# Optimization experiments

Measured on AMD Instinct MI355X. Metric: run time of the kernel, lower is better.

## Reference

```python
import jax, jax.numpy as jnp
import numpy as np

N_NODES = 50000
FEAT = 128
FP_LEN = 2048
RADIUS = 4
N_EDGES = 600000
BN_EPS = 1e-5


def setup_inputs() -> dict:
    key = jax.random.key(0)
    ks = jax.random.split(key, 8)
    s_h = 1.0 / np.sqrt(FEAT)  # torch Linear default init scale
    return {
        "atoms_features": jax.random.normal(ks[0], (N_NODES, FEAT), jnp.float32),
        "edge_index": jax.random.randint(ks[1], (2, N_EDGES), 0, N_NODES, dtype=jnp.int64),
        "init_w": jax.random.normal(ks[2], (FEAT, FP_LEN), jnp.float32) * s_h,
        "init_b": jnp.zeros((FP_LEN,), jnp.float32),
        "hash_w": jax.random.normal(ks[3], (RADIUS, FEAT, FEAT), jnp.float32) * s_h,
        "hash_b": jnp.zeros((RADIUS, FEAT), jnp.float32),
        "soft_w": jax.random.normal(ks[4], (RADIUS, FEAT, FP_LEN), jnp.float32) * s_h,
        "soft_b": jnp.zeros((RADIUS, FP_LEN), jnp.float32),
        "bn_gamma": jnp.ones((FEAT,), jnp.float32),
        "bn_beta": jnp.zeros((FEAT,), jnp.float32),
    }


def reference(atoms_features, edge_index, init_w, init_b, hash_w, hash_b,
              soft_w, soft_b, bn_gamma, bn_beta):
    n = atoms_features.shape[0]
    src, dst = edge_index[0], edge_index[1]

    # initial soft assignment: fingerprint += sum_atoms softmax(W x + b)
    fp = jnp.sum(jax.nn.softmax(atoms_features @ init_w + init_b, axis=1), axis=0)

    feats = atoms_features
    for l in range(RADIUS):
        # neighbor-sum aggregation: self + sum of neighbor features (scatter-add over edges)
        agg = feats + jax.ops.segment_sum(feats[src], dst, num_segments=n)
        # hash: Linear -> ReLU -> BatchNorm (training-mode batch stats, biased var)
        h = jax.nn.relu(agg @ hash_w[l] + hash_b[l])
        mu = jnp.mean(h, axis=0)
        var = jnp.mean(jnp.square(h - mu), axis=0)
        h = (h - mu) * jax.lax.rsqrt(var + BN_EPS) * bn_gamma + bn_beta
        # soft assignment contribution
        fp = fp + jnp.sum(jax.nn.softmax(h @ soft_w[l] + soft_b[l], axis=1), axis=0)
        # original round-trips through numpy between layers -> detach
        feats = jax.lax.stop_gradient(h)

    return fp[None, :]  # [1, FP_LEN]
```

## Files before the change

kernel.cpp:

```cpp
#include <hip/hip_runtime.h>
#include <hip/hip_bf16.h>

#define N_NODES 50000
#define FEAT    128
#define FP_LEN  2048
#define RADIUS  4
#define N_EDGES 600000
#define BN_EPS  1e-5f
#define SM_ROWS 16

__global__ __launch_bounds__(256) void k_zero(float* fp, float* stats,
                                              int* counts, int* cursor) {
    int i = blockIdx.x * blockDim.x + threadIdx.x;
    int n = gridDim.x * blockDim.x;
    for (int j = i; j < FP_LEN; j += n) fp[j] = 0.f;
    for (int j = i; j < RADIUS * 2 * FEAT; j += n) stats[j] = 0.f;
    for (int j = i; j < N_NODES; j += n) { counts[j] = 0; cursor[j] = 0; }
}

__global__ __launch_bounds__(256) void k_count(const int* __restrict__ dst,
                                               int* __restrict__ counts) {
    int e = blockIdx.x * 256 + threadIdx.x;
    if (e < N_EDGES) {
        unsigned d = (unsigned)dst[e];
        if (d < N_NODES) atomicAdd(&counts[d], 1);
    }
}

__global__ __launch_bounds__(1024) void k_scan(const int* __restrict__ counts,
                                               int* __restrict__ offs) {
    __shared__ int part[1024];
    int tid = threadIdx.x;
    const int chunk = (N_NODES + 1023) / 1024;
    int lo = tid * chunk;
    int hi = min(lo + chunk, N_NODES);
    int s = 0;
    for (int i = lo; i < hi; i++) s += counts[i];
    part[tid] = s;
    __syncthreads();
    for (int off = 1; off < 1024; off <<= 1) {
        int v = (tid >= off) ? part[tid - off] : 0;
        __syncthreads();
        part[tid] += v;
        __syncthreads();
    }
    int run = part[tid] - s;
    for (int i = lo; i < hi; i++) { offs[i] = run; run += counts[i]; }
    if (lo < N_NODES && hi == N_NODES) offs[N_NODES] = run;
}

__global__ __launch_bounds__(256) void k_fill(const int* __restrict__ src,
                                              const int* __restrict__ dst,
                                              const int* __restrict__ offs,
                                              int* __restrict__ cursor,
                                              int* __restrict__ csr) {
    int e = blockIdx.x * 256 + threadIdx.x;
    if (e < N_EDGES) {
        unsigned d = (unsigned)dst[e];
        unsigned s = (unsigned)src[e];
        if (d < N_NODES && s < N_NODES) {
            int p = atomicAdd(&cursor[d], 1);
            csr[offs[d] + p] = (int)s;
        }
    }
}

__global__ __launch_bounds__(256) void k_agg(const float* __restrict__ feats,
                                             float* __restrict__ agg,
                                             const int* __restrict__ offs,
                                             const int* __restrict__ csr) {
    int node = blockIdx.x * 4 + (threadIdx.x >> 6);
    int lane = threadIdx.x & 63;
    const float2* f2 = (const float2*)feats;
    float2 acc = f2[node * 64 + lane];
    int j0 = offs[node], j1 = offs[node + 1];
    for (int j = j0; j < j1; j++) {
        int s = csr[j];
        float2 v = f2[s * 64 + lane];
        acc.x += v.x; acc.y += v.y;
    }
    ((float2*)agg)[node * 64 + lane] = acc;
}

__global__ __launch_bounds__(256) void k_hash(const float* __restrict__ agg,
                                              const float* __restrict__ W,
                                              const float* __restrict__ bias,
                                              float* __restrict__ h,
                                              float* __restrict__ stat_sum,
                                              float* __restrict__ stat_sq) {
    __shared__ float Alds[64 * 128];
    int t = threadIdx.x;
    int row0 = blockIdx.x * 64;

    const float4* A4 = (const float4*)(agg + (size_t)row0 * FEAT);
    float4* L4 = (float4*)Alds;
    #pragma unroll
    for (int i = 0; i < 8; i++) {
        int idx = t + i * 256;
        int r = idx >> 5;
        if (row0 + r < N_NODES) L4[idx] = A4[idx];
        else L4[idx] = make_float4(0.f, 0.f, 0.f, 0.f);
    }
    __syncthreads();

    int cg = t & 63;
    int rg = t >> 6;
    int c0 = cg * 2;

    float acc[16][2];
    #pragma unroll
    for (int r = 0; r < 16; r++) { acc[r][0] = 0.f; acc[r][1] = 0.f; }

    #pragma unroll 4
    for (int kk = 0; kk < FEAT; kk++) {
        float2 b = ((const float2*)(W + (size_t)kk * FEAT))[cg];
        #pragma unroll
        for (int r = 0; r < 16; r++) {
            float a = Alds[(rg * 16 + r) * FEAT + kk];
            acc[r][0] += a * b.x;
            acc[r][1] += a * b.y;
        }
    }

    float b0 = bias[c0], b1 = bias[c0 + 1];
    float ps0 = 0.f, ps1 = 0.f, pq0 = 0.f, pq1 = 0.f;
    float2* H2 = (float2*)h;
    #pragma unroll
    for (int r = 0; r < 16; r++) {
        int row = row0 + rg * 16 + r;
        if (row < N_NODES) {
            float v0 = fmaxf(acc[r][0] + b0, 0.f);
            float v1 = fmaxf(acc[r][1] + b1, 0.f);
            H2[(size_t)row * 64 + cg] = make_float2(v0, v1);
            ps0 += v0; ps1 += v1;
            pq0 += v0 * v0; pq1 += v1 * v1;
        }
    }

    __syncthreads();
    float* red = Alds;
    red[rg * FEAT + c0]     = ps0;
    red[rg * FEAT + c0 + 1] = ps1;
    red[512 + rg * FEAT + c0]     = pq0;
    red[512 + rg * FEAT + c0 + 1] = pq1;
    __syncthreads();
    if (t < FEAT) {
        float s = red[t] + red[FEAT + t] + red[2 * FEAT + t] + red[3 * FEAT + t];
        float q = red[512 + t] + red[512 + FEAT + t] + red[512 + 2 * FEAT + t] +
                  red[512 + 3 * FEAT + t];
        atomicAdd(&stat_sum[t], s);
        atomicAdd(&stat_sq[t], q);
    }
}

__global__ void k_finalize(float* stat_sum, float* stat_sq,
                           const float* __restrict__ gamma,
                           const float* __restrict__ beta) {
    int c = threadIdx.x;
    float mu = stat_sum[c] * (1.f / N_NODES);
    float var = stat_sq[c] * (1.f / N_NODES) - mu * mu;
    float sc = gamma[c] * rsqrtf(var + BN_EPS);
    float sh = beta[c] - mu * sc;
    stat_sum[c] = sc;
    stat_sq[c] = sh;
}

__global__ __launch_bounds__(256) void k_bnapply(float* __restrict__ h,
                                                 const float* __restrict__ scale,
                                                 const float* __restrict__ shift) {
    int i = blockIdx.x * 256 + threadIdx.x;
    const float4* sc4 = (const float4*)scale;
    const float4* sh4 = (const float4*)shift;
    if (i < N_NODES * 32) {
        float4 v = ((float4*)h)[i];
        int cb = i & 31;
        float4 s = sc4[cb], b = sh4[cb];
        v.x = v.x * s.x + b.x;
        v.y = v.y * s.y + b.y;
        v.z = v.z * s.z + b.z;
        v.w = v.w * s.w + b.w;
        ((float4*)h)[i] = v;
    }
}

__global__ __launch_bounds__(256) void k_smgemm(const float* __restrict__ X,
                                                const float* __restrict__ W,
                                                const float* __restrict__ bias,
                                                float* __restrict__ fp) {
    __shared__ float Alds[SM_ROWS * FEAT];
    __shared__ float red[4 * SM_ROWS];
    int t = threadIdx.x;
    int row0 = blockIdx.x * SM_ROWS;

    const float4* X4 = (const float4*)(X + (size_t)row0 * FEAT);
    ((float4*)Alds)[t]       = X4[t];
    ((float4*)Alds)[256 + t] = X4[256 + t];
    __syncthreads();

    float L[SM_ROWS][8];
    #pragma unroll
    for (int r = 0; r < SM_ROWS; r++)
        #pragma unroll
        for (int c = 0; c < 8; c++) L[r][c] = 0.f;

    const float4* W4 = (const float4*)W;
    float4 nb0 = W4[t];
    float4 nb1 = W4[256 + t];
    for (int kk = 0; kk < FEAT; kk++) {
        float4 b0 = nb0, b1 = nb1;
        int nk = (kk + 1) & 127;
        nb0 = W4[(size_t)nk * 512 + t];
        nb1 = W4[(size_t)nk * 512 + 256 + t];
        float a[SM_ROWS];
        #pragma unroll
        for (int r = 0; r < SM_ROWS; r++) a[r] = Alds[r * FEAT + kk];
        #pragma unroll
        for (int r = 0; r < SM_ROWS; r++) {
            L[r][0] += a[r] * b0.x; L[r][1] += a[r] * b0.y;
            L[r][2] += a[r] * b0.z; L[r][3] += a[r] * b0.w;
            L[r][4] += a[r] * b1.x; L[r][5] += a[r] * b1.y;
            L[r][6] += a[r] * b1.z; L[r][7] += a[r] * b1.w;
        }
    }

    float4 bb0 = ((const float4*)bias)[t];
    float4 bb1 = ((const float4*)bias)[256 + t];
    #pragma unroll
    for (int r = 0; r < SM_ROWS; r++) {
        L[r][0] += bb0.x; L[r][1] += bb0.y; L[r][2] += bb0.z; L[r][3] += bb0.w;
        L[r][4] += bb1.x; L[r][5] += bb1.y; L[r][6] += bb1.z; L[r][7] += bb1.w;
    }

    int wave = t >> 6, lane = t & 63;

    float m[SM_ROWS];
    #pragma unroll
    for (int r = 0; r < SM_ROWS; r++) {
        float tm = L[r][0];
        #pragma unroll
        for (int c = 1; c < 8; c++) tm = fmaxf(tm, L[r][c]);
        #pragma unroll
        for (int off = 32; off >= 1; off >>= 1)
            tm = fmaxf(tm, __shfl_xor(tm, off));
        if (lane == 0) red[wave * SM_ROWS + r] = tm;
    }
    __syncthreads();
    #pragma unroll
    for (int r = 0; r < SM_ROWS; r++)
        m[r] = fmaxf(fmaxf(red[r], red[SM_ROWS + r]),
                     fmaxf(red[2 * SM_ROWS + r], red[3 * SM_ROWS + r]));
    __syncthreads();

    float invZ[SM_ROWS];
    #pragma unroll
    for (int r = 0; r < SM_ROWS; r++) {
        float s = 0.f;
        #pragma unroll
        for (int c = 0; c < 8; c++) {
            L[r][c] = __expf(L[r][c] - m[r]);
            s += L[r][c];
        }
        #pragma unroll
        for (int off = 32; off >= 1; off >>= 1)
            s += __shfl_xor(s, off);
        if (lane == 0) red[wave * SM_ROWS + r] = s;
    }
    __syncthreads();
    #pragma unroll
    for (int r = 0; r < SM_ROWS; r++) {
        float Z = red[r] + red[SM_ROWS + r] + red[2 * SM_ROWS + r] +
                  red[3 * SM_ROWS + r];
        invZ[r] = 1.f / Z;
    }

    #pragma unroll
    for (int c = 0; c < 4; c++) {
        float v = 0.f;
        #pragma unroll
        for (int r = 0; r < SM_ROWS; r++) v += L[r][c] * invZ[r];
        atomicAdd(&fp[t * 4 + c], v);
    }
    #pragma unroll
    for (int c = 4; c < 8; c++) {
        float v = 0.f;
        #pragma unroll
        for (int r = 0; r < SM_ROWS; r++) v += L[r][c] * invZ[r];
        atomicAdd(&fp[1024 + t * 4 + (c - 4)], v);
    }
}

extern "C" void kernel_launch(void* const* d_in, const int* in_sizes, int n_in,
                              void* d_out, int out_size, void* d_ws, size_t ws_size,
                              hipStream_t stream) {
    const float* atoms  = (const float*)d_in[0];
    const int*   eidx   = (const int*)d_in[1];
    const float* init_w = (const float*)d_in[2];
    const float* init_b = (const float*)d_in[3];
    const float* hash_w = (const float*)d_in[4];
    const float* hash_b = (const float*)d_in[5];
    const float* soft_w = (const float*)d_in[6];
    const float* soft_b = (const float*)d_in[7];
    const float* gamma  = (const float*)d_in[8];
    const float* beta   = (const float*)d_in[9];
    float* fp = (float*)d_out;

    char* ws = (char*)d_ws;
    float* F      = (float*)ws; ws += (size_t)N_NODES * FEAT * 4;
    float* A      = (float*)ws; ws += (size_t)N_NODES * FEAT * 4;
    int*   counts = (int*)ws;   ws += (size_t)N_NODES * 4;
    int*   cursor = (int*)ws;   ws += (size_t)N_NODES * 4;
    int*   offs   = (int*)ws;   ws += (size_t)(N_NODES + 4) * 4;
    int*   csr    = (int*)ws;   ws += (size_t)N_EDGES * 4;
    float* stats  = (float*)ws; ws += (size_t)RADIUS * 2 * FEAT * 4;

    const int* src = eidx;
    const int* dst = eidx + N_EDGES;

    k_zero<<<256, 256, 0, stream>>>(fp, stats, counts, cursor);
    k_count<<<(N_EDGES + 255) / 256, 256, 0, stream>>>(dst, counts);
    k_scan<<<1, 1024, 0, stream>>>(counts, offs);
    k_fill<<<(N_EDGES + 255) / 256, 256, 0, stream>>>(src, dst, offs, cursor, csr);

    k_smgemm<<<N_NODES / SM_ROWS, 256, 0, stream>>>(atoms, init_w, init_b, fp);

    const float* feats = atoms;
    for (int l = 0; l < RADIUS; l++) {
        k_agg<<<N_NODES / 4, 256, 0, stream>>>(feats, A, offs, csr);
        float* ss = stats + l * 2 * FEAT;
        float* sq = ss + FEAT;
        k_hash<<<(N_NODES + 63) / 64, 256, 0, stream>>>(
            A, hash_w + (size_t)l * FEAT * FEAT, hash_b + (size_t)l * FEAT,
            F, ss, sq);
        k_finalize<<<1, FEAT, 0, stream>>>(ss, sq, gamma, beta);
        k_bnapply<<<(N_NODES * 32 + 255) / 256, 256, 0, stream>>>(F, ss, sq);
        k_smgemm<<<N_NODES / SM_ROWS, 256, 0, stream>>>(
            F, soft_w + (size_t)l * FEAT * FP_LEN, soft_b + (size_t)l * FP_LEN, fp);
        feats = F;
    }
}
```

Measured before the change: 2.927 ms.

## Use split-bf16 MFMA for hash and softmax GEMMs with pre-transposed weights

Replaces the FP32 FMA GEMMs in the hash layer and the soft-assignment/softmax kernel with bf16 MFMA instructions. Each operand is split into hi and lo parts and three products are summed to keep close to FP32 accuracy. Weights are split and transposed once per call into workspace, and activations are split into a swizzled LDS layout. The softmax kernel grows to 32 rows per block and accumulates column sums in LDS before doing global atomics. This costs an extra weight-conversion kernel and triple MFMA work, and carries some precision risk.

```diff
diff --git a/kernel.cpp b/kernel.cpp
--- a/kernel.cpp
+++ b/kernel.cpp
@@ -7,7 +7,44 @@
 #define RADIUS  4
 #define N_EDGES 600000
 #define BN_EPS  1e-5f
-#define SM_ROWS 16
+
+typedef __attribute__((ext_vector_type(8))) short bh8;
+typedef __attribute__((ext_vector_type(4))) float f32x4;
+
+__device__ __forceinline__ unsigned bf16_rne(float x) {
+    unsigned u = __float_as_uint(x);
+    return (u + 0x7fffu + ((u >> 16) & 1u)) >> 16;
+}
+
+__device__ __forceinline__ void split2(float x0, float x1, unsigned& hi, unsigned& lo) {
+    unsigned h0 = bf16_rne(x0), h1 = bf16_rne(x1);
+    float r0 = x0 - __uint_as_float(h0 << 16);
+    float r1 = x1 - __uint_as_float(h1 << 16);
+    hi = h0 | (h1 << 16);
+    lo = bf16_rne(r0) | (bf16_rne(r1) << 16);
+}
+
+template <int ROWS, int NT>
+__device__ __forceinline__ void stage_split(const float* __restrict__ X, int row0,
+                                            unsigned short* Ahi, unsigned short* Alo,
+                                            int t) {
+    const int NF4 = ROWS * 32;
+    const float4* X4 = (const float4*)(X + (size_t)row0 * FEAT);
+    #pragma unroll
+    for (int f = t; f < NF4; f += NT) {
+        int row = f >> 5, kq = f & 31;
+        float4 v = make_float4(0.f, 0.f, 0.f, 0.f);
+        if (row0 + row < N_NODES) v = X4[f];
+        unsigned h0, l0, h1, l1;
+        split2(v.x, v.y, h0, l0);
+        split2(v.z, v.w, h1, l1);
+        int boff = (kq * 8) ^ ((row & 7) << 4);
+        unsigned* dh = (unsigned*)((char*)Ahi + row * 256 + boff);
+        unsigned* dl = (unsigned*)((char*)Alo + row * 256 + boff);
+        dh[0] = h0; dh[1] = h1;
+        dl[0] = l0; dl[1] = l1;
+    }
+}
 
 __global__ __launch_bounds__(256) void k_zero(float* fp, float* stats,
                                               int* counts, int* cursor) {
@@ -16,6 +53,57 @@
     for (int j = i; j < FP_LEN; j += n) fp[j] = 0.f;
     for (int j = i; j < RADIUS * 2 * FEAT; j += n) stats[j] = 0.f;
     for (int j = i; j < N_NODES; j += n) { counts[j] = 0; cursor[j] = 0; }
+}
+
+__global__ __launch_bounds__(256) void k_wsplit(
+    const float* __restrict__ init_w, const float* __restrict__ soft_w,
+    const float* __restrict__ hash_w,
+    unsigned* __restrict__ WhiB, unsigned* __restrict__ WloB,
+    unsigned* __restrict__ WhiH, unsigned* __restrict__ WloH) {
+    __shared__ float Tl[128][65];
+    int t = threadIdx.x;
+    int y = blockIdx.y;
+    const float* W;
+    unsigned *Oh, *Ol;
+    int N;
+    if (y < 5) {
+        N = FP_LEN;
+        W = (y == 0) ? init_w : soft_w + (size_t)(y - 1) * FEAT * FP_LEN;
+        Oh = WhiB + (size_t)y * FP_LEN * (FEAT / 2);
+        Ol = WloB + (size_t)y * FP_LEN * (FEAT / 2);
+    } else {
+        if (blockIdx.x >= 2) return;
+        N = FEAT;
+        W = hash_w + (size_t)(y - 5) * FEAT * FEAT;
+        Oh = WhiH + (size_t)(y - 5) * FEAT * (FEAT / 2);
+        Ol = WloH + (size_t)(y - 5) * FEAT * (FEAT / 2);
+    }
+    int n0 = blockIdx.x * 64;
+    #pragma unroll
+    for (int i = 0; i < 8; i++) {
+        int f = t + i * 256;
+        int k = f >> 4, nq = f & 15;
+        float4 v = *(const float4*)(W + (size_t)k * N + n0 + nq * 4);
+        Tl[k][nq * 4 + 0] = v.x; Tl[k][nq * 4 + 1] = v.y;
+        Tl[k][nq * 4 + 2] = v.z; Tl[k][nq * 4 + 3] = v.w;
+    }
+    __syncthreads();
+    int nl = t >> 2, kq = t & 3;
+    unsigned hi[16], lo[16];
+    #pragma unroll
+    for (int d = 0; d < 16; d++) {
+        float x0 = Tl[kq * 32 + 2 * d][nl];
+        float x1 = Tl[kq * 32 + 2 * d + 1][nl];
+        split2(x0, x1, hi[d], lo[d]);
+    }
+    size_t col = n0 + nl;
+    uint4* H = (uint4*)Oh + col * 16 + kq * 4;
+    uint4* L = (uint4*)Ol + col * 16 + kq * 4;
+    #pragma unroll
+    for (int j = 0; j < 4; j++) {
+        H[j] = make_uint4(hi[4 * j], hi[4 * j + 1], hi[4 * j + 2], hi[4 * j + 3]);
+        L[j] = make_uint4(lo[4 * j], lo[4 * j + 1], lo[4 * j + 2], lo[4 * j + 3]);
+    }
 }
 
 __global__ __launch_bounds__(256) void k_count(const int* __restrict__ dst,
@@ -82,74 +170,73 @@
     ((float2*)agg)[node * 64 + lane] = acc;
 }
 
-__global__ __launch_bounds__(256) void k_hash(const float* __restrict__ agg,
-                                              const float* __restrict__ W,
-                                              const float* __restrict__ bias,
-                                              float* __restrict__ h,
-                                              float* __restrict__ stat_sum,
-                                              float* __restrict__ stat_sq) {
-    __shared__ float Alds[64 * 128];
+__global__ __launch_bounds__(256) void k_hash_mfma(
+    const float* __restrict__ Xagg,
+    const unsigned* __restrict__ WhiT, const unsigned* __restrict__ WloT,
+    const float* __restrict__ bias, float* __restrict__ h,
+    float* __restrict__ stat_sum, float* __restrict__ stat_sq) {
+    __shared__ unsigned short Ahi[64 * FEAT];
+    __shared__ unsigned short Alo[64 * FEAT];
+    __shared__ float colred[2][4][FEAT];
+
     int t = threadIdx.x;
     int row0 = blockIdx.x * 64;
-
-    const float4* A4 = (const float4*)(agg + (size_t)row0 * FEAT);
-    float4* L4 = (float4*)Alds;
-    #pragma unroll
-    for (int i = 0; i < 8; i++) {
-        int idx = t + i * 256;
-        int r = idx >> 5;
-        if (row0 + r < N_NODES) L4[idx] = A4[idx];
-        else L4[idx] = make_float4(0.f, 0.f, 0.f, 0.f);
-    }
-    __syncthreads();
-
-    int cg = t & 63;
-    int rg = t >> 6;
-    int c0 = cg * 2;
-
-    float acc[16][2];
-    #pragma unroll
-    for (int r = 0; r < 16; r++) { acc[r][0] = 0.f; acc[r][1] = 0.f; }
-
-    #pragma unroll 4
-    for (int kk = 0; kk < FEAT; kk++) {
-        float2 b = ((const float2*)(W + (size_t)kk * FEAT))[cg];
-        #pragma unroll
-        for (int r = 0; r < 16; r++) {
-            float a = Alds[(rg * 16 + r) * FEAT + kk];
-            acc[r][0] += a * b.x;
-            acc[r][1] += a * b.y;
-        }
-    }
-
-    float b0 = bias[c0], b1 = bias[c0 + 1];
-    float ps0 = 0.f, ps1 = 0.f, pq0 = 0.f, pq1 = 0.f;
-    float2* H2 = (float2*)h;
-    #pragma unroll
-    for (int r = 0; r < 16; r++) {
-        int row = row0 + rg * 16 + r;
-        if (row < N_NODES) {
-            float v0 = fmaxf(acc[r][0] + b0, 0.f);
-            float v1 = fmaxf(acc[r][1] + b1, 0.f);
-            H2[(size_t)row * 64 + cg] = make_float2(v0, v1);
-            ps0 += v0; ps1 += v1;
-            pq0 += v0 * v0; pq1 += v1 * v1;
-        }
-    }
-
-    __syncthreads();
-    float* red = Alds;
-    red[rg * FEAT + c0]     = ps0;
-    red[rg * FEAT + c0 + 1] = ps1;
-    red[512 + rg * FEAT + c0]     = pq0;
-    red[512 + rg * FEAT + c0 + 1] = pq1;
+    stage_split<64, 256>(Xagg, row0, Ahi, Alo, t);
+    __syncthreads();
+
+    int wave = t >> 6, lane = t & 63;
+    int g = lane >> 4, q = lane & 15;
+
+    f32x4 acc[8];
+    #pragma unroll
+    for (int n = 0; n < 8; n++) acc[n] = (f32x4){0.f, 0.f, 0.f, 0.f};
+
+    int arow = wave * 16 + q;
+    const uint4* BH = (const uint4*)WhiT;
+    const uint4* BL = (const uint4*)WloT;
+
+    for (int s = 0; s < 4; s++) {
+        int aoff = arow * 256 + (((s * 64) + (g * 16)) ^ ((arow & 7) << 4));
+        bh8 ah = *(const bh8*)((const char*)Ahi + aoff);
+        bh8 al = *(const bh8*)((const char*)Alo + aoff);
+        #pragma unroll
+        for (int n = 0; n < 8; n++) {
+            int idx = (n * 16 + q) * 16 + s * 4 + g;
+            bh8 bhf = __builtin_bit_cast(bh8, BH[idx]);
+            bh8 blf = __builtin_bit_cast(bh8, BL[idx]);
+            acc[n] = __builtin_amdgcn_mfma_f32_16x16x32_bf16(ah, bhf, acc[n], 0, 0, 0);
+            acc[n] = __builtin_amdgcn_mfma_f32_16x16x32_bf16(ah, blf, acc[n], 0, 0, 0);
+            acc[n] = __builtin_amdgcn_mfma_f32_16x16x32_bf16(al, bhf, acc[n], 0, 0, 0);
+        }
+    }
+
+    float vmask[4];
+    #pragma unroll
+    for (int j = 0; j < 4; j++)
+        vmask[j] = (row0 + wave * 16 + g * 4 + j < N_NODES) ? 1.f : 0.f;
+    #pragma unroll
+    for (int n = 0; n < 8; n++) {
+        int col = n * 16 + q;
+        float b = bias[col];
+        float cs = 0.f, cq = 0.f;
+        #pragma unroll
+        for (int j = 0; j < 4; j++) {
+            float v = fmaxf(acc[n][j] + b, 0.f) * vmask[j];
+            if (vmask[j] != 0.f)
+                h[(size_t)(row0 + wave * 16 + g * 4 + j) * FEAT + col] = v;
+            cs += v; cq += v * v;
+        }
+        cs += __shfl_xor(cs, 16); cs += __shfl_xor(cs, 32);
+        cq += __shfl_xor(cq, 16); cq += __shfl_xor(cq, 32);
+        if (g == 0) { colred[0][wave][col] = cs; colred[1][wave][col] = cq; }
+    }
     __syncthreads();
     if (t < FEAT) {
-        float s = red[t] + red[FEAT + t] + red[2 * FEAT + t] + red[3 * FEAT + t];
-        float q = red[512 + t] + red[512 + FEAT + t] + red[512 + 2 * FEAT + t] +
-                  red[512 + 3 * FEAT + t];
+        float s = 0.f, qq = 0.f;
+        #pragma unroll
+        for (int w2 = 0; w2 < 4; w2++) { s += colred[0][w2][t]; qq += colred[1][w2][t]; }
         atomicAdd(&stat_sum[t], s);
-        atomicAdd(&stat_sq[t], q);
+        atomicAdd(&stat_sq[t], qq);
     }
 }
 
@@ -183,109 +270,127 @@
     }
 }
 
-__global__ __launch_bounds__(256) void k_smgemm(const float* __restrict__ X,
-                                                const float* __restrict__ W,
-                                                const float* __restrict__ bias,
-                                                float* __restrict__ fp) {
-    __shared__ float Alds[SM_ROWS * FEAT];
-    __shared__ float red[4 * SM_ROWS];
+__global__ __launch_bounds__(512) void k_smgemm_mfma(
+    const float* __restrict__ X,
+    const unsigned* __restrict__ WhiT, const unsigned* __restrict__ WloT,
+    const float* __restrict__ bias, float* __restrict__ fp) {
+    __shared__ unsigned short Ahi[32 * FEAT];
+    __shared__ unsigned short Alo[32 * FEAT];
+    __shared__ float fpacc[FP_LEN];
+    __shared__ float red[32 * 4];
+
     int t = threadIdx.x;
-    int row0 = blockIdx.x * SM_ROWS;
-
-    const float4* X4 = (const float4*)(X + (size_t)row0 * FEAT);
-    ((float4*)Alds)[t]       = X4[t];
-    ((float4*)Alds)[256 + t] = X4[256 + t];
-    __syncthreads();
-
-    float L[SM_ROWS][8];
-    #pragma unroll
-    for (int r = 0; r < SM_ROWS; r++)
-        #pragma unroll
-        for (int c = 0; c < 8; c++) L[r][c] = 0.f;
-
-    const float4* W4 = (const float4*)W;
-    float4 nb0 = W4[t];
-    float4 nb1 = W4[256 + t];
-    for (int kk = 0; kk < FEAT; kk++) {
-        float4 b0 = nb0, b1 = nb1;
-        int nk = (kk + 1) & 127;
-        nb0 = W4[(size_t)nk * 512 + t];
-        nb1 = W4[(size_t)nk * 512 + 256 + t];
-        float a[SM_ROWS];
-        #pragma unroll
-        for (int r = 0; r < SM_ROWS; r++) a[r] = Alds[r * FEAT + kk];
-        #pragma unroll
-        for (int r = 0; r < SM_ROWS; r++) {
-            L[r][0] += a[r] * b0.x; L[r][1] += a[r] * b0.y;
-            L[r][2] += a[r] * b0.z; L[r][3] += a[r] * b0.w;
-            L[r][4] += a[r] * b1.x; L[r][5] += a[r] * b1.y;
-            L[r][6] += a[r] * b1.z; L[r][7] += a[r] * b1.w;
-        }
-    }
-
-    float4 bb0 = ((const float4*)bias)[t];
-    float4 bb1 = ((const float4*)bias)[256 + t];
-    #pragma unroll
-    for (int r = 0; r < SM_ROWS; r++) {
-        L[r][0] += bb0.x; L[r][1] += bb0.y; L[r][2] += bb0.z; L[r][3] += bb0.w;
-        L[r][4] += bb1.x; L[r][5] += bb1.y; L[r][6] += bb1.z; L[r][7] += bb1.w;
-    }
+    int row0 = blockIdx.x * 32;
+
+    #pragma unroll
+    for (int i = 0; i < 4; i++) fpacc[t + i * 512] = 0.f;
+
+    stage_split<32, 512>(X, row0, Ahi, Alo, t);
+    __syncthreads();
 
     int wave = t >> 6, lane = t & 63;
-
-    float m[SM_ROWS];
-    #pragma unroll
-    for (int r = 0; r < SM_ROWS; r++) {
-        float tm = L[r][0];
-        #pragma unroll
-        for (int c = 1; c < 8; c++) tm = fmaxf(tm, L[r][c]);
-        #pragma unroll
-        for (int off = 32; off >= 1; off >>= 1)
-            tm = fmaxf(tm, __shfl_xor(tm, off));
-        if (lane == 0) red[wave * SM_ROWS + r] = tm;
-    }
-    __syncthreads();
-    #pragma unroll
-    for (int r = 0; r < SM_ROWS; r++)
-        m[r] = fmaxf(fmaxf(red[r], red[SM_ROWS + r]),
-                     fmaxf(red[2 * SM_ROWS + r], red[3 * SM_ROWS + r]));
-    __syncthreads();
-
-    float invZ[SM_ROWS];
-    #pragma unroll
-    for (int r = 0; r < SM_ROWS; r++) {
-        float s = 0.f;
-        #pragma unroll
-        for (int c = 0; c < 8; c++) {
-            L[r][c] = __expf(L[r][c] - m[r]);
-            s += L[r][c];
-        }
-        #pragma unroll
-        for (int off = 32; off >= 1; off >>= 1)
-            s += __shfl_xor(s, off);
-        if (lane == 0) red[wave * SM_ROWS + r] = s;
-    }
-    __syncthreads();
-    #pragma unroll
-    for (int r = 0; r < SM_ROWS; r++) {
-        float Z = red[r] + red[SM_ROWS + r] + red[2 * SM_ROWS + r] +
-                  red[3 * SM_ROWS + r];
-        invZ[r] = 1.f / Z;
-    }
-
-    #pragma unroll
-    for (int c = 0; c < 4; c++) {
-        float v = 0.f;
-        #pragma unroll
-        for (int r = 0; r < SM_ROWS; r++) v += L[r][c] * invZ[r];
-        atomicAdd(&fp[t * 4 + c], v);
-    }
-    #pragma unroll
-    for (int c = 4; c < 8; c++) {
-        float v = 0.f;
-        #pragma unroll
-        for (int r = 0; r < SM_ROWS; r++) v += L[r][c] * invZ[r];
-        atomicAdd(&fp[1024 + t * 4 + (c - 4)], v);
+    int rg = wave >> 2, cg = wave & 3;
+    int g = lane >> 4, q = lane & 15;
+
+    f32x4 acc[32];
+    #pragma unroll
+    for (int n = 0; n < 32; n++) acc[n] = (f32x4){0.f, 0.f, 0.f, 0.f};
+
+    int arow = rg * 16 + q;
+    const uint4* BH = (const uint4*)WhiT;
+    const uint4* BL = (const uint4*)WloT;
+    int bbase = (cg * 512 + q) * 16 + g;
+
+    for (int s = 0; s < 4; s++) {
+        int aoff = arow * 256 + (((s * 64) + (g * 16)) ^ ((arow & 7) << 4));
+        bh8 ah = *(const bh8*)((const char*)Ahi + aoff);
+        bh8 al = *(const bh8*)((const char*)Alo + aoff);
+        int base = bbase + s * 4;
+        uint4 bh = BH[base], bl = BL[base];
+        #pragma unroll
+        for (int n = 0; n < 32; n++) {
+            uint4 bhc = bh, blc = bl;
+            if (n < 31) { bh = BH[base + (n + 1) * 256]; bl = BL[base + (n + 1) * 256]; }
+            bh8 bhf = __builtin_bit_cast(bh8, bhc);
+            bh8 blf = __builtin_bit_cast(bh8, blc);
+            acc[n] = __builtin_amdgcn_mfma_f32_16x16x32_bf16(ah, bhf, acc[n], 0, 0, 0);
+            acc[n] = __builtin_amdgcn_mfma_f32_16x16x32_bf16(ah, blf, acc[n], 0, 0, 0);
+            acc[n] = __builtin_amdgcn_mfma_f32_16x16x32_bf16(al, bhf, acc[n], 0, 0, 0);
+        }
+    }
+
+    int colb = cg * 512 + q;
+    float m[4] = {-3.4e38f, -3.4e38f, -3.4e38f, -3.4e38f};
+    #pragma unroll
+    for (int n = 0; n < 32; n++) {
+        float b = bias[colb + n * 16];
+        #pragma unroll
+        for (int j = 0; j < 4; j++) {
+            acc[n][j] += b;
+            m[j] = fmaxf(m[j], acc[n][j]);
+        }
+    }
+    #pragma unroll
+    for (int j = 0; j < 4; j++) {
+        m[j] = fmaxf(m[j], __shfl_xor(m[j], 1));
+        m[j] = fmaxf(m[j], __shfl_xor(m[j], 2));
+        m[j] = fmaxf(m[j], __shfl_xor(m[j], 4));
+        m[j] = fmaxf(m[j], __shfl_xor(m[j], 8));
+    }
+    if (q == 0) {
+        #pragma unroll
+        for (int j = 0; j < 4; j++) red[(rg * 16 + g * 4 + j) * 4 + cg] = m[j];
+    }
+    __syncthreads();
+    #pragma unroll
+    for (int j = 0; j < 4; j++) {
+        const float* r = &red[(rg * 16 + g * 4 + j) * 4];
+        m[j] = fmaxf(fmaxf(r[0], r[1]), fmaxf(r[2], r[3]));
+    }
+    __syncthreads();
+
+    float sm[4] = {0.f, 0.f, 0.f, 0.f};
+    #pragma unroll
+    for (int n = 0; n < 32; n++)
+        #pragma unroll
+        for (int j = 0; j < 4; j++) {
+            float e = __expf(acc[n][j] - m[j]);
+            acc[n][j] = e;
+            sm[j] += e;
+        }
+    #pragma unroll
+    for (int j = 0; j < 4; j++) {
+        sm[j] += __shfl_xor(sm[j], 1);
+        sm[j] += __shfl_xor(sm[j], 2);
+        sm[j] += __shfl_xor(sm[j], 4);
+        sm[j] += __shfl_xor(sm[j], 8);
+    }
+    if (q == 0) {
+        #pragma unroll
+        for (int j = 0; j < 4; j++) red[(rg * 16 + g * 4 + j) * 4 + cg] = sm[j];
+    }
+    __syncthreads();
+    float invZ[4];
+    #pragma unroll
+    for (int j = 0; j < 4; j++) {
+        const float* r = &red[(rg * 16 + g * 4 + j) * 4];
+        float Z = r[0] + r[1] + r[2] + r[3];
+        float vm = (row0 + rg * 16 + g * 4 + j < N_NODES) ? 1.f : 0.f;
+        invZ[j] = vm / Z;
+    }
+    #pragma unroll
+    for (int n = 0; n < 32; n++) {
+        float c = acc[n][0] * invZ[0] + acc[n][1] * invZ[1] +
+                  acc[n][2] * invZ[2] + acc[n][3] * invZ[3];
+        c += __shfl_xor(c, 16);
+        c += __shfl_xor(c, 32);
+        if (g == 0) atomicAdd(&fpacc[colb + n * 16], c);
+    }
+    __syncthreads();
+    #pragma unroll
+    for (int i = 0; i < 4; i++) {
+        int cidx = t + i * 512;
+        atomicAdd(&fp[cidx], fpacc[cidx]);
     }
 }
 
@@ -312,29 +417,41 @@
     int*   offs   = (int*)ws;   ws += (size_t)(N_NODES + 4) * 4;
     int*   csr    = (int*)ws;   ws += (size_t)N_EDGES * 4;
     float* stats  = (float*)ws; ws += (size_t)RADIUS * 2 * FEAT * 4;
+    unsigned* WhiB = (unsigned*)ws; ws += (size_t)5 * FP_LEN * (FEAT / 2) * 4;
+    unsigned* WloB = (unsigned*)ws; ws += (size_t)5 * FP_LEN * (FEAT / 2) * 4;
+    unsigned* WhiH = (unsigned*)ws; ws += (size_t)RADIUS * FEAT * (FEAT / 2) * 4;
+    unsigned* WloH = (unsigned*)ws; ws += (size_t)RADIUS * FEAT * (FEAT / 2) * 4;
 
     const int* src = eidx;
     const int* dst = eidx + N_EDGES;
 
     k_zero<<<256, 256, 0, stream>>>(fp, stats, counts, cursor);
+    k_wsplit<<<dim3(32, 9), 256, 0, stream>>>(init_w, soft_w, hash_w,
+                                              WhiB, WloB, WhiH, WloH);
     k_count<<<(N_EDGES + 255) / 256, 256, 0, stream>>>(dst, counts);
     k_scan<<<1, 1024, 0, stream>>>(counts, offs);
     k_fill<<<(N_EDGES + 255) / 256, 256, 0, stream>>>(src, dst, offs, cursor, csr);
 
-    k_smgemm<<<N_NODES / SM_ROWS, 256, 0, stream>>>(atoms, init_w, init_b, fp);
+    const int SMG = (N_NODES + 31) / 32;
+    const int HG  = (N_NODES + 63) / 64;
+
+    k_smgemm_mfma<<<SMG, 512, 0, stream>>>(atoms, WhiB, WloB, init_b, fp);
 
     const float* feats = atoms;
     for (int l = 0; l < RADIUS; l++) {
         k_agg<<<N_NODES / 4, 256, 0, stream>>>(feats, A, offs, csr);
         float* ss = stats + l * 2 * FEAT;
         float* sq = ss + FEAT;
-        k_hash<<<(N_NODES + 63) / 64, 256, 0, stream>>>(
-            A, hash_w + (size_t)l * FEAT * FEAT, hash_b + (size_t)l * FEAT,
-            F, ss, sq);
+        k_hash_mfma<<<HG, 256, 0, stream>>>(
+            A, WhiH + (size_t)l * FEAT * (FEAT / 2),
+            WloH + (size_t)l * FEAT * (FEAT / 2),
+            hash_b + (size_t)l * FEAT, F, ss, sq);
         k_finalize<<<1, FEAT, 0, stream>>>(ss, sq, gamma, beta);
         k_bnapply<<<(N_NODES * 32 + 255) / 256, 256, 0, stream>>>(F, ss, sq);
-        k_smgemm<<<N_NODES / SM_ROWS, 256, 0, stream>>>(
-            F, soft_w + (size_t)l * FEAT * FP_LEN, soft_b + (size_t)l * FP_LEN, fp);
+        k_smgemm_mfma<<<SMG, 512, 0, stream>>>(
+            F, WhiB + (size_t)(1 + l) * FP_LEN * (FEAT / 2),
+            WloB + (size_t)(1 + l) * FP_LEN * (FEAT / 2),
+            soft_b + (size_t)l * FP_LEN, fp);
         feats = F;
     }
 }
```

Result: slower. 3.299 ms (+12.7%).
